# Kernel tuning notes

Hardware: AMD Instinct MI355X
Metric: run time of the kernel (lower is better)

Reference implementation:

```python
import jax, jax.numpy as jnp
import numpy as np

D = 512
H = 8
HD = D // H
EPS = 1e-8


def setup_inputs() -> dict:
    key = jax.random.key(0)
    ks = jax.random.split(key, 16)
    B, S = 4, 2048
    s = lambda n: 1.0 / np.sqrt(n)
    inp = {
        "gene_emb": jax.random.normal(ks[0], (B, S, D), jnp.float32),
        "expr_emb": jax.random.normal(ks[1], (B, S, D), jnp.float32),
        "M": jax.random.uniform(ks[2], (B, S, S), jnp.float32),
        # weights stored (in, out) so y = x @ W + b
        "W_fused": jax.random.normal(ks[3], (2 * D, D), jnp.float32) * s(2 * D),
        "b_fused": jnp.zeros((D,), jnp.float32),
        "W_Q": jax.random.normal(ks[4], (D, D), jnp.float32) * s(D),
        "b_Q": jnp.zeros((D,), jnp.float32),
        "W_K": jax.random.normal(ks[5], (D, D), jnp.float32) * s(D),
        "b_K": jnp.zeros((D,), jnp.float32),
        "W_V": jax.random.normal(ks[6], (D, D), jnp.float32) * s(D),
        "b_V": jnp.zeros((D,), jnp.float32),
        "W_O": jax.random.normal(ks[7], (D, D), jnp.float32) * s(D),
        "b_O": jnp.zeros((D,), jnp.float32),
    }
    return inp


def reference(gene_emb, expr_emb, M, W_fused, b_fused, W_Q, b_Q, W_K, b_K, W_V, b_V, W_O, b_O):
    B, S, _ = gene_emb.shape
    scale = HD ** (-0.5)
    fused = jnp.concatenate([gene_emb, expr_emb], axis=-1) @ W_fused + b_fused
    # (B,S,D) -> (B,H,S,HD)
    split = lambda x: x.reshape(B, S, H, HD).transpose(0, 2, 1, 3)
    Q = split(fused @ W_Q + b_Q)
    K = split(fused @ W_K + b_K)
    V = split(expr_emb @ W_V + b_V)
    scores = jnp.einsum("bhqd,bhkd->bhqk", Q, K) * scale
    Mg = M[:, None, :, :]  # broadcast over heads
    scores = scores * Mg
    attn = jax.nn.softmax(scores, axis=-1)
    A_sparse = attn * Mg
    norm = jnp.sum(jnp.abs(A_sparse), axis=-1, keepdims=True) + EPS
    A_bar = A_sparse / norm
    out = jnp.einsum("bhqk,bhkd->bhqd", A_bar, V)
    out = out.transpose(0, 2, 1, 3).reshape(B, S, D)
    return out @ W_O + b_O
```

## Files before the change

kernel.cpp:

```cpp
#include <hip/hip_runtime.h>

typedef unsigned short u16;
typedef __attribute__((ext_vector_type(8))) short bf16x8_t;
typedef __attribute__((ext_vector_type(4))) float f32x4_t;

__device__ __forceinline__ u16 f2bf(float x){
  union { float f; unsigned u; } v; v.f = x;
  unsigned r = v.u + 0x7FFFu + ((v.u >> 16) & 1u);
  return (u16)(r >> 16);
}
__device__ __forceinline__ float bf2f(u16 h){
  union { unsigned u; float f; } v; v.u = ((unsigned)h) << 16;
  return v.f;
}

__device__ __forceinline__ void gl2lds16(const u16* g, u16* l){
  __builtin_amdgcn_global_load_lds((const __attribute__((address_space(1))) void*)g,
                                   (__attribute__((address_space(3))) void*)l, 16, 0, 0);
}

__global__ __launch_bounds__(256) void split_concat_kernel(
    const float* __restrict__ gene, const float* __restrict__ expr,
    u16* __restrict__ Xh, u16* __restrict__ Xl)
{
  size_t e = ((size_t)blockIdx.x * 256 + threadIdx.x) * 4;
  int row = (int)(e >> 10);
  int col = (int)(e & 1023);
  const float* src = (col < 512) ? (gene + (size_t)row * 512 + col)
                                 : (expr + (size_t)row * 512 + (col - 512));
  float4 v = *(const float4*)src;
  float a[4] = {v.x, v.y, v.z, v.w};
  u16 hs[4], ls[4];
#pragma unroll
  for (int i = 0; i < 4; i++){
    hs[i] = f2bf(a[i]);
    ls[i] = f2bf(a[i] - bf2f(hs[i]));
  }
  *(uint2*)(Xh + e) = make_uint2(hs[0] | ((unsigned)hs[1] << 16), hs[2] | ((unsigned)hs[3] << 16));
  *(uint2*)(Xl + e) = make_uint2(ls[0] | ((unsigned)ls[1] << 16), ls[2] | ((unsigned)ls[3] << 16));
}

__global__ __launch_bounds__(256) void transpose_split_kernel(
    const float* __restrict__ W, u16* __restrict__ Wth, u16* __restrict__ Wtl,
    int K, int N)
{
  __shared__ float t[64][65];
  int k0 = blockIdx.x * 64, n0 = blockIdx.y * 64;
  int tid = threadIdx.x;
  int r = tid >> 4;
  int c4 = (tid & 15) * 4;
#pragma unroll
  for (int p = 0; p < 4; p++){
    int k = p * 16 + r;
    float4 v = *(const float4*)(W + (size_t)(k0 + k) * N + n0 + c4);
    t[c4 + 0][k] = v.x; t[c4 + 1][k] = v.y; t[c4 + 2][k] = v.z; t[c4 + 3][k] = v.w;
  }
  __syncthreads();
#pragma unroll
  for (int p = 0; p < 4; p++){
    int n = p * 16 + r;
    u16 hs[4], ls[4];
#pragma unroll
    for (int i = 0; i < 4; i++){
      float x = t[n][c4 + i];
      hs[i] = f2bf(x);
      ls[i] = f2bf(x - bf2f(hs[i]));
    }
    size_t o = (size_t)(n0 + n) * K + k0 + c4;
    *(uint2*)(Wth + o) = make_uint2(hs[0] | ((unsigned)hs[1] << 16), hs[2] | ((unsigned)hs[3] << 16));
    *(uint2*)(Wtl + o) = make_uint2(ls[0] | ((unsigned)ls[1] << 16), ls[2] | ((unsigned)ls[3] << 16));
  }
}

__global__ __launch_bounds__(256, 2) void gemm_split_kernel(
    const u16* __restrict__ Ah, const u16* __restrict__ Al, int lda,
    const u16* __restrict__ Bth, const u16* __restrict__ Btl, int K,
    const float* __restrict__ bias,
    void* __restrict__ out0, void* __restrict__ out1, int mode)
{
  __shared__ __align__(16) u16 sAh[128 * 32], sAl[128 * 32];
  __shared__ __align__(16) u16 sBh[64 * 32],  sBl[64 * 32];
  int tid = threadIdx.x;
  int lane = tid & 63, w = tid >> 6, quad = lane >> 4, l15 = lane & 15;
  int wm = w & 1, wn = w >> 1;
  int m0 = blockIdx.x * 128, n0 = blockIdx.y * 64;

  f32x4_t acc[4][2];
#pragma unroll
  for (int i = 0; i < 4; i++)
#pragma unroll
    for (int j = 0; j < 2; j++)
#pragma unroll
      for (int r = 0; r < 4; r++) acc[i][j][r] = 0.f;

  int lrow = lane >> 2;
  int swzS = ((lane >> 2) & 3) ^ ((lane >> 4) & 3);
  int gkq  = ((lane & 3) ^ swzS) * 8;
  const u16* pAh0 = Ah + (size_t)(m0 + w * 32 + lrow) * lda + gkq;
  const u16* pAh1 = Ah + (size_t)(m0 + w * 32 + 16 + lrow) * lda + gkq;
  const u16* pAl0 = Al + (size_t)(m0 + w * 32 + lrow) * lda + gkq;
  const u16* pAl1 = Al + (size_t)(m0 + w * 32 + 16 + lrow) * lda + gkq;
  const u16* pBh0 = Bth + (size_t)(n0 + w * 16 + lrow) * K + gkq;
  const u16* pBl0 = Btl + (size_t)(n0 + w * 16 + lrow) * K + gkq;
  u16* dAh = sAh + w * 1024;
  u16* dAl = sAl + w * 1024;
  u16* dBh = sBh + w * 512;
  u16* dBl = sBl + w * 512;

  int pq = (quad ^ ((l15 & 3) ^ ((l15 >> 2) & 3))) * 8;

  for (int k0 = 0; k0 < K; k0 += 32){
    __syncthreads();
    gl2lds16(pAh0 + k0, dAh);
    gl2lds16(pAh1 + k0, dAh + 512);
    gl2lds16(pAl0 + k0, dAl);
    gl2lds16(pAl1 + k0, dAl + 512);
    gl2lds16(pBh0 + k0, dBh);
    gl2lds16(pBl0 + k0, dBl);
    __syncthreads();

    bf16x8_t aH[4], aL[4], bH[2], bL[2];
#pragma unroll
    for (int mi = 0; mi < 4; mi++){
      int ad = (wm * 64 + mi * 16 + l15) * 32 + pq;
      aH[mi] = *(const bf16x8_t*)&sAh[ad];
      aL[mi] = *(const bf16x8_t*)&sAl[ad];
    }
#pragma unroll
    for (int ni = 0; ni < 2; ni++){
      int bd = (wn * 32 + ni * 16 + l15) * 32 + pq;
      bH[ni] = *(const bf16x8_t*)&sBh[bd];
      bL[ni] = *(const bf16x8_t*)&sBl[bd];
    }
#pragma unroll
    for (int mi = 0; mi < 4; mi++)
#pragma unroll
      for (int ni = 0; ni < 2; ni++){
        acc[mi][ni] = __builtin_amdgcn_mfma_f32_16x16x32_bf16(aH[mi], bH[ni], acc[mi][ni], 0, 0, 0);
        acc[mi][ni] = __builtin_amdgcn_mfma_f32_16x16x32_bf16(aH[mi], bL[ni], acc[mi][ni], 0, 0, 0);
        acc[mi][ni] = __builtin_amdgcn_mfma_f32_16x16x32_bf16(aL[mi], bH[ni], acc[mi][ni], 0, 0, 0);
      }
  }

#pragma unroll
  for (int mi = 0; mi < 4; mi++)
#pragma unroll
    for (int ni = 0; ni < 2; ni++){
      int gn = n0 + wn * 32 + ni * 16 + l15;
      float bs = bias[gn];
      int gm0 = m0 + wm * 64 + mi * 16 + quad * 4;
#pragma unroll
      for (int r = 0; r < 4; r++){
        float v = acc[mi][ni][r] + bs;
        int gm = gm0 + r;
        if (mode == 0){
          u16 hb = f2bf(v);
          ((u16*)out0)[(size_t)gm * 512 + gn] = hb;
          ((u16*)out1)[(size_t)gm * 512 + gn] = f2bf(v - bf2f(hb));
        } else if (mode == 1){
          int bb = gm >> 11, s = gm & 2047;
          int hh = gn >> 6, d = gn & 63;
          ((u16*)out0)[((size_t)((bb * 8 + hh) * 64 + d) << 11) + s] = f2bf(v);
        } else {
          ((float*)out0)[(size_t)gm * 512 + gn] = v;
        }
      }
    }
}

__global__ __launch_bounds__(256, 4) void flash_kernel(
    const u16* __restrict__ Qh, const u16* __restrict__ Ql,
    const u16* __restrict__ Kh, const u16* __restrict__ Kl,
    const u16* __restrict__ Vt, const float* __restrict__ Mm,
    u16* __restrict__ Oh, u16* __restrict__ Ol)
{
  __shared__ __align__(16) u16 sKh[64 * 64], sKl[64 * 64], sVt[64 * 64];
  __shared__ __align__(16) u16 sP[64 * 72];
  int tid = threadIdx.x, lane = tid & 63, w = tid >> 6, quad = lane >> 4, l15 = lane & 15;
  int bh = blockIdx.y, b = bh >> 3, h = bh & 7;
  int q0 = blockIdx.x * 64;
  const float scale = 0.125f;

  int qrow = q0 + w * 16 + l15;
  const u16* qpH = Qh + ((size_t)(b * 2048 + qrow)) * 512 + h * 64 + quad * 8;
  const u16* qpL = Ql + ((size_t)(b * 2048 + qrow)) * 512 + h * 64 + quad * 8;
  bf16x8_t qH[2], qL[2];
  qH[0] = *(const bf16x8_t*)qpH;  qH[1] = *(const bf16x8_t*)(qpH + 32);
  qL[0] = *(const bf16x8_t*)qpL;  qL[1] = *(const bf16x8_t*)(qpL + 32);

  float lp[4] = {0.f, 0.f, 0.f, 0.f};
  f32x4_t Oacc[4];
#pragma unroll
  for (int ni = 0; ni < 4; ni++)
#pragma unroll
    for (int r = 0; r < 4; r++) Oacc[ni][r] = 0.f;

  int srow = lane >> 3;
  int gc = ((lane & 7) ^ ((lane >> 3) & 7)) * 8;
  const u16* gKh0 = Kh + ((size_t)(b * 2048 + w * 16 + srow)) * 512 + h * 64 + gc;
  const u16* gKl0 = Kl + ((size_t)(b * 2048 + w * 16 + srow)) * 512 + h * 64 + gc;
  const u16* gVt0 = Vt + ((size_t)(bh * 64 + w * 16 + srow)) * 2048 + gc;
  u16* dKh = sKh + w * 1024;
  u16* dKl = sKl + w * 1024;
  u16* dVt = sVt + w * 1024;
  const float* Mbase = Mm + (size_t)b * 2048 * 2048 + (size_t)(q0 + w * 16) * 2048;

  int sw7 = l15 & 7;
  for (int k0 = 0; k0 < 2048; k0 += 64){
    __syncthreads();
    gl2lds16(gKh0 + (size_t)k0 * 512,        dKh);
    gl2lds16(gKh0 + (size_t)(k0 + 8) * 512,  dKh + 512);
    gl2lds16(gKl0 + (size_t)k0 * 512,        dKl);
    gl2lds16(gKl0 + (size_t)(k0 + 8) * 512,  dKl + 512);
    gl2lds16(gVt0 + k0,                      dVt);
    gl2lds16(gVt0 + 8 * 2048 + k0,           dVt + 512);
    __syncthreads();

    float Mv[4][4];
#pragma unroll
    for (int ni = 0; ni < 4; ni++)
#pragma unroll
      for (int r = 0; r < 4; r++)
        Mv[ni][r] = Mbase[(size_t)(quad * 4 + r) * 2048 + k0 + ni * 16 + l15];

    f32x4_t Sacc[4];
#pragma unroll
    for (int ni = 0; ni < 4; ni++)
#pragma unroll
      for (int r = 0; r < 4; r++) Sacc[ni][r] = 0.f;
#pragma unroll
    for (int ni = 0; ni < 4; ni++){
      int kb = (ni * 16 + l15) * 64;
#pragma unroll
      for (int ds = 0; ds < 2; ds++){
        int p = ((ds * 4 + quad) ^ sw7) * 8;
        bf16x8_t kH = *(const bf16x8_t*)&sKh[kb + p];
        bf16x8_t kL = *(const bf16x8_t*)&sKl[kb + p];
        Sacc[ni] = __builtin_amdgcn_mfma_f32_16x16x32_bf16(qH[ds], kH, Sacc[ni], 0, 0, 0);
        Sacc[ni] = __builtin_amdgcn_mfma_f32_16x16x32_bf16(qH[ds], kL, Sacc[ni], 0, 0, 0);
        Sacc[ni] = __builtin_amdgcn_mfma_f32_16x16x32_bf16(qL[ds], kH, Sacc[ni], 0, 0, 0);
      }
    }

#pragma unroll
    for (int ni = 0; ni < 4; ni++)
#pragma unroll
      for (int r = 0; r < 4; r++){
        float m = Mv[ni][r];
        float p = m * __expf(Sacc[ni][r] * scale * m);
        lp[r] += p;
        sP[(w * 16 + quad * 4 + r) * 72 + ni * 16 + l15] = f2bf(p);
      }

#pragma unroll
    for (int ds = 0; ds < 2; ds++){
      bf16x8_t pf = *(const bf16x8_t*)&sP[(w * 16 + l15) * 72 + ds * 32 + quad * 8];
#pragma unroll
      for (int ni = 0; ni < 4; ni++){
        int p = ((ds * 4 + quad) ^ sw7) * 8;
        bf16x8_t vf = *(const bf16x8_t*)&sVt[(ni * 16 + l15) * 64 + p];
        Oacc[ni] = __builtin_amdgcn_mfma_f32_16x16x32_bf16(pf, vf, Oacc[ni], 0, 0, 0);
      }
    }
  }

#pragma unroll
  for (int r = 0; r < 4; r++){
#pragma unroll
    for (int off = 1; off < 16; off <<= 1)
      lp[r] += __shfl_xor(lp[r], off);
  }

#pragma unroll
  for (int r = 0; r < 4; r++){
    float inv = 1.0f / lp[r];
    int q = q0 + w * 16 + quad * 4 + r;
    size_t rb = ((size_t)(b * 2048 + q)) * 512 + h * 64;
#pragma unroll
    for (int ni = 0; ni < 4; ni++){
      float v = Oacc[ni][r] * inv;
      int d = ni * 16 + l15;
      u16 hb = f2bf(v);
      Oh[rb + d] = hb;
      Ol[rb + d] = f2bf(v - bf2f(hb));
    }
  }
}

extern "C" void kernel_launch(void* const* d_in, const int* in_sizes, int n_in,
                              void* d_out, int out_size, void* d_ws, size_t ws_size,
                              hipStream_t stream)
{
  const float* gene = (const float*)d_in[0];
  const float* expr = (const float*)d_in[1];
  const float* Mm   = (const float*)d_in[2];
  const float* Wf   = (const float*)d_in[3];
  const float* bfv  = (const float*)d_in[4];
  const float* Wq   = (const float*)d_in[5];
  const float* bq   = (const float*)d_in[6];
  const float* Wk   = (const float*)d_in[7];
  const float* bk   = (const float*)d_in[8];
  const float* Wv   = (const float*)d_in[9];
  const float* bv   = (const float*)d_in[10];
  const float* Wo   = (const float*)d_in[11];
  const float* bo   = (const float*)d_in[12];
  float* out = (float*)d_out;

  char* ws = (char*)d_ws;
  size_t off = 0;
  auto alloc = [&](size_t bytes) -> void* {
    void* p = (void*)(ws + off);
    off += (bytes + 255) & ~(size_t)255;
    return p;
  };
  u16* Xh   = (u16*)alloc(8192ull * 1024 * 2);
  u16* Xl   = (u16*)alloc(8192ull * 1024 * 2);
  u16* Wfth = (u16*)alloc(512ull * 1024 * 2);
  u16* Wftl = (u16*)alloc(512ull * 1024 * 2);
  u16* Wqth = (u16*)alloc(512ull * 512 * 2);
  u16* Wqtl = (u16*)alloc(512ull * 512 * 2);
  u16* Wkth = (u16*)alloc(512ull * 512 * 2);
  u16* Wktl = (u16*)alloc(512ull * 512 * 2);
  u16* Wvth = (u16*)alloc(512ull * 512 * 2);
  u16* Wvtl = (u16*)alloc(512ull * 512 * 2);
  u16* Woth = (u16*)alloc(512ull * 512 * 2);
  u16* Wotl = (u16*)alloc(512ull * 512 * 2);
  u16* Fh   = (u16*)alloc(8192ull * 512 * 2);
  u16* Fl   = (u16*)alloc(8192ull * 512 * 2);
  u16* Qh   = (u16*)alloc(8192ull * 512 * 2);
  u16* Ql   = (u16*)alloc(8192ull * 512 * 2);
  u16* Kh   = (u16*)alloc(8192ull * 512 * 2);
  u16* Kl   = (u16*)alloc(8192ull * 512 * 2);
  u16* Vt   = (u16*)alloc(8192ull * 512 * 2);
  u16* Oh = Xh;
  u16* Ol = Xl;

  split_concat_kernel<<<8192, 256, 0, stream>>>(gene, expr, Xh, Xl);
  transpose_split_kernel<<<dim3(16, 8), 256, 0, stream>>>(Wf, Wfth, Wftl, 1024, 512);
  transpose_split_kernel<<<dim3(8, 8),  256, 0, stream>>>(Wq, Wqth, Wqtl, 512, 512);
  transpose_split_kernel<<<dim3(8, 8),  256, 0, stream>>>(Wk, Wkth, Wktl, 512, 512);
  transpose_split_kernel<<<dim3(8, 8),  256, 0, stream>>>(Wv, Wvth, Wvtl, 512, 512);
  transpose_split_kernel<<<dim3(8, 8),  256, 0, stream>>>(Wo, Woth, Wotl, 512, 512);

  gemm_split_kernel<<<dim3(64, 8), 256, 0, stream>>>(Xh, Xl, 1024, Wfth, Wftl, 1024, bfv, Fh, Fl, 0);
  gemm_split_kernel<<<dim3(64, 8), 256, 0, stream>>>(Fh, Fl, 512, Wqth, Wqtl, 512, bq, Qh, Ql, 0);
  gemm_split_kernel<<<dim3(64, 8), 256, 0, stream>>>(Fh, Fl, 512, Wkth, Wktl, 512, bk, Kh, Kl, 0);
  gemm_split_kernel<<<dim3(64, 8), 256, 0, stream>>>(Xh + 512, Xl + 512, 1024, Wvth, Wvtl, 512, bv, Vt, nullptr, 1);
  flash_kernel<<<dim3(32, 32), 256, 0, stream>>>(Qh, Ql, Kh, Kl, Vt, Mm, Oh, Ol);
  gemm_split_kernel<<<dim3(64, 8), 256, 0, stream>>>(Oh, Ol, 512, Woth, Wotl, 512, bo, out, nullptr, 2);

  (void)in_sizes; (void)n_in; (void)out_size; (void)ws_size;
}
```

Measured before the change: 372.9 us.

## Drop split-bf16 terms, fuse Q/K GEMMs and weight transposes, prefetch mask

Cuts the compensated bf16 splitting in stages that tolerate it. Q/K and V/O GEMMs drop the low weight parts, the output projection becomes single bf16, and the attention QK^T uses one MFMA instead of three. The five weight transposes are merged into one launch, and Q and K are computed in one dual GEMM with the softmax scale and log2(e) folded into Q so exp2 can be used. The mask tile is now prefetched one iteration ahead, and P is truncated instead of rounded. All of this lowers MFMA count, memory traffic and launch overhead at the cost of accuracy.

Result: faster. 301.7 us (-19.1%).

```diff
diff --git a/kernel.cpp b/kernel.cpp
--- a/kernel.cpp
+++ b/kernel.cpp
@@ -12,6 +12,10 @@
 __device__ __forceinline__ float bf2f(u16 h){
   union { unsigned u; float f; } v; v.u = ((unsigned)h) << 16;
   return v.f;
+}
+__device__ __forceinline__ u16 hi16(float x){
+  union { float f; unsigned u; } v; v.f = x;
+  return (u16)(v.u >> 16);
 }
 
 __device__ __forceinline__ void gl2lds16(const u16* g, u16* l){
@@ -40,19 +44,32 @@
   *(uint2*)(Xl + e) = make_uint2(ls[0] | ((unsigned)ls[1] << 16), ls[2] | ((unsigned)ls[3] << 16));
 }
 
-__global__ __launch_bounds__(256) void transpose_split_kernel(
-    const float* __restrict__ W, u16* __restrict__ Wth, u16* __restrict__ Wtl,
-    int K, int N)
+__global__ __launch_bounds__(256) void transpose_all_kernel(
+    const float* __restrict__ Wf, const float* __restrict__ Wq,
+    const float* __restrict__ Wk, const float* __restrict__ Wv,
+    const float* __restrict__ Wo,
+    u16* __restrict__ Wfth, u16* __restrict__ Wftl,
+    u16* __restrict__ Wqth, u16* __restrict__ Wkth,
+    u16* __restrict__ Wvth, u16* __restrict__ Woth)
 {
   __shared__ float t[64][65];
-  int k0 = blockIdx.x * 64, n0 = blockIdx.y * 64;
+  int id = blockIdx.x;
+  const float* W; u16* Th; u16* Tl; int K, kx, ny;
+  if (id < 128){ W = Wf; Th = Wfth; Tl = Wftl; K = 1024; kx = id >> 3; ny = id & 7; }
+  else {
+    int tt = id - 128; int wi = tt >> 6; tt &= 63; kx = tt >> 3; ny = tt & 7; K = 512;
+    W  = (wi == 0) ? Wq  : (wi == 1) ? Wk  : (wi == 2) ? Wv  : Wo;
+    Th = (wi == 0) ? Wqth: (wi == 1) ? Wkth: (wi == 2) ? Wvth: Woth;
+    Tl = nullptr;
+  }
+  int k0 = kx * 64, n0 = ny * 64;
   int tid = threadIdx.x;
   int r = tid >> 4;
   int c4 = (tid & 15) * 4;
 #pragma unroll
   for (int p = 0; p < 4; p++){
     int k = p * 16 + r;
-    float4 v = *(const float4*)(W + (size_t)(k0 + k) * N + n0 + c4);
+    float4 v = *(const float4*)(W + (size_t)(k0 + k) * 512 + n0 + c4);
     t[c4 + 0][k] = v.x; t[c4 + 1][k] = v.y; t[c4 + 2][k] = v.z; t[c4 + 3][k] = v.w;
   }
   __syncthreads();
@@ -67,23 +84,35 @@
       ls[i] = f2bf(x - bf2f(hs[i]));
     }
     size_t o = (size_t)(n0 + n) * K + k0 + c4;
-    *(uint2*)(Wth + o) = make_uint2(hs[0] | ((unsigned)hs[1] << 16), hs[2] | ((unsigned)hs[3] << 16));
-    *(uint2*)(Wtl + o) = make_uint2(ls[0] | ((unsigned)ls[1] << 16), ls[2] | ((unsigned)ls[3] << 16));
-  }
-}
-
-__global__ __launch_bounds__(256, 2) void gemm_split_kernel(
+    *(uint2*)(Th + o) = make_uint2(hs[0] | ((unsigned)hs[1] << 16), hs[2] | ((unsigned)hs[3] << 16));
+    if (Tl)
+      *(uint2*)(Tl + o) = make_uint2(ls[0] | ((unsigned)ls[1] << 16), ls[2] | ((unsigned)ls[3] << 16));
+  }
+}
+
+template<int SPLITS, int MODE, int DUAL>
+__global__ __launch_bounds__(256, 2) void gemm_kernel(
     const u16* __restrict__ Ah, const u16* __restrict__ Al, int lda,
-    const u16* __restrict__ Bth, const u16* __restrict__ Btl, int K,
-    const float* __restrict__ bias,
-    void* __restrict__ out0, void* __restrict__ out1, int mode)
-{
-  __shared__ __align__(16) u16 sAh[128 * 32], sAl[128 * 32];
-  __shared__ __align__(16) u16 sBh[64 * 32],  sBl[64 * 32];
+    const u16* __restrict__ Bh0, const u16* __restrict__ Bl0,
+    const u16* __restrict__ Bh1, int K,
+    const float* __restrict__ bias0, const float* __restrict__ bias1,
+    void* __restrict__ out0, void* __restrict__ out1, void* __restrict__ outsec,
+    float sc0, float sc1)
+{
+  __shared__ __align__(16) u16 sAh[128 * 32];
+  __shared__ __align__(16) u16 sAl[SPLITS >= 2 ? 128 * 32 : 8];
+  __shared__ __align__(16) u16 sBh[64 * 32];
+  __shared__ __align__(16) u16 sBl[SPLITS == 3 ? 64 * 32 : 8];
   int tid = threadIdx.x;
   int lane = tid & 63, w = tid >> 6, quad = lane >> 4, l15 = lane & 15;
   int wm = w & 1, wn = w >> 1;
-  int m0 = blockIdx.x * 128, n0 = blockIdx.y * 64;
+  int m0 = blockIdx.x * 128;
+  int side = DUAL ? (int)(blockIdx.y >> 3) : 0;
+  int n0 = (DUAL ? (int)(blockIdx.y & 7) : (int)blockIdx.y) * 64;
+  const u16* Bh = (DUAL && side) ? Bh1 : Bh0;
+  const float* bias = (DUAL && side) ? bias1 : bias0;
+  void* o0 = (DUAL && side) ? outsec : out0;
+  float sc = (DUAL && side) ? sc1 : sc0;
 
   f32x4_t acc[4][2];
 #pragma unroll
@@ -98,10 +127,10 @@
   int gkq  = ((lane & 3) ^ swzS) * 8;
   const u16* pAh0 = Ah + (size_t)(m0 + w * 32 + lrow) * lda + gkq;
   const u16* pAh1 = Ah + (size_t)(m0 + w * 32 + 16 + lrow) * lda + gkq;
-  const u16* pAl0 = Al + (size_t)(m0 + w * 32 + lrow) * lda + gkq;
-  const u16* pAl1 = Al + (size_t)(m0 + w * 32 + 16 + lrow) * lda + gkq;
-  const u16* pBh0 = Bth + (size_t)(n0 + w * 16 + lrow) * K + gkq;
-  const u16* pBl0 = Btl + (size_t)(n0 + w * 16 + lrow) * K + gkq;
+  const u16* pAl0 = (SPLITS >= 2) ? Al + (size_t)(m0 + w * 32 + lrow) * lda + gkq : nullptr;
+  const u16* pAl1 = (SPLITS >= 2) ? Al + (size_t)(m0 + w * 32 + 16 + lrow) * lda + gkq : nullptr;
+  const u16* pBh0 = Bh + (size_t)(n0 + w * 16 + lrow) * K + gkq;
+  const u16* pBl0 = (SPLITS == 3) ? Bl0 + (size_t)(n0 + w * 16 + lrow) * K + gkq : nullptr;
   u16* dAh = sAh + w * 1024;
   u16* dAl = sAl + w * 1024;
   u16* dBh = sBh + w * 512;
@@ -113,10 +142,13 @@
     __syncthreads();
     gl2lds16(pAh0 + k0, dAh);
     gl2lds16(pAh1 + k0, dAh + 512);
-    gl2lds16(pAl0 + k0, dAl);
-    gl2lds16(pAl1 + k0, dAl + 512);
+    if constexpr (SPLITS >= 2){
+      gl2lds16(pAl0 + k0, dAl);
+      gl2lds16(pAl1 + k0, dAl + 512);
+    }
     gl2lds16(pBh0 + k0, dBh);
-    gl2lds16(pBl0 + k0, dBl);
+    if constexpr (SPLITS == 3)
+      gl2lds16(pBl0 + k0, dBl);
     __syncthreads();
 
     bf16x8_t aH[4], aL[4], bH[2], bL[2];
@@ -124,21 +156,23 @@
     for (int mi = 0; mi < 4; mi++){
       int ad = (wm * 64 + mi * 16 + l15) * 32 + pq;
       aH[mi] = *(const bf16x8_t*)&sAh[ad];
-      aL[mi] = *(const bf16x8_t*)&sAl[ad];
+      if constexpr (SPLITS >= 2) aL[mi] = *(const bf16x8_t*)&sAl[ad];
     }
 #pragma unroll
     for (int ni = 0; ni < 2; ni++){
       int bd = (wn * 32 + ni * 16 + l15) * 32 + pq;
       bH[ni] = *(const bf16x8_t*)&sBh[bd];
-      bL[ni] = *(const bf16x8_t*)&sBl[bd];
+      if constexpr (SPLITS == 3) bL[ni] = *(const bf16x8_t*)&sBl[bd];
     }
 #pragma unroll
     for (int mi = 0; mi < 4; mi++)
 #pragma unroll
       for (int ni = 0; ni < 2; ni++){
         acc[mi][ni] = __builtin_amdgcn_mfma_f32_16x16x32_bf16(aH[mi], bH[ni], acc[mi][ni], 0, 0, 0);
-        acc[mi][ni] = __builtin_amdgcn_mfma_f32_16x16x32_bf16(aH[mi], bL[ni], acc[mi][ni], 0, 0, 0);
-        acc[mi][ni] = __builtin_amdgcn_mfma_f32_16x16x32_bf16(aL[mi], bH[ni], acc[mi][ni], 0, 0, 0);
+        if constexpr (SPLITS == 3)
+          acc[mi][ni] = __builtin_amdgcn_mfma_f32_16x16x32_bf16(aH[mi], bL[ni], acc[mi][ni], 0, 0, 0);
+        if constexpr (SPLITS >= 2)
+          acc[mi][ni] = __builtin_amdgcn_mfma_f32_16x16x32_bf16(aL[mi], bH[ni], acc[mi][ni], 0, 0, 0);
       }
   }
 
@@ -153,40 +187,38 @@
       for (int r = 0; r < 4; r++){
         float v = acc[mi][ni][r] + bs;
         int gm = gm0 + r;
-        if (mode == 0){
+        if constexpr (MODE == 0){
           u16 hb = f2bf(v);
-          ((u16*)out0)[(size_t)gm * 512 + gn] = hb;
+          ((u16*)o0)[(size_t)gm * 512 + gn] = hb;
           ((u16*)out1)[(size_t)gm * 512 + gn] = f2bf(v - bf2f(hb));
-        } else if (mode == 1){
+        } else if constexpr (MODE == 1){
+          ((u16*)o0)[(size_t)gm * 512 + gn] = f2bf(v * sc);
+        } else if constexpr (MODE == 2){
           int bb = gm >> 11, s = gm & 2047;
           int hh = gn >> 6, d = gn & 63;
-          ((u16*)out0)[((size_t)((bb * 8 + hh) * 64 + d) << 11) + s] = f2bf(v);
+          ((u16*)o0)[((size_t)((bb * 8 + hh) * 64 + d) << 11) + s] = f2bf(v);
         } else {
-          ((float*)out0)[(size_t)gm * 512 + gn] = v;
+          ((float*)o0)[(size_t)gm * 512 + gn] = v;
         }
       }
     }
 }
 
 __global__ __launch_bounds__(256, 4) void flash_kernel(
-    const u16* __restrict__ Qh, const u16* __restrict__ Ql,
-    const u16* __restrict__ Kh, const u16* __restrict__ Kl,
+    const u16* __restrict__ Qh, const u16* __restrict__ Kh,
     const u16* __restrict__ Vt, const float* __restrict__ Mm,
-    u16* __restrict__ Oh, u16* __restrict__ Ol)
-{
-  __shared__ __align__(16) u16 sKh[64 * 64], sKl[64 * 64], sVt[64 * 64];
+    u16* __restrict__ Oh)
+{
+  __shared__ __align__(16) u16 sKh[64 * 64], sVt[64 * 64];
   __shared__ __align__(16) u16 sP[64 * 72];
   int tid = threadIdx.x, lane = tid & 63, w = tid >> 6, quad = lane >> 4, l15 = lane & 15;
   int bh = blockIdx.y, b = bh >> 3, h = bh & 7;
   int q0 = blockIdx.x * 64;
-  const float scale = 0.125f;
 
   int qrow = q0 + w * 16 + l15;
-  const u16* qpH = Qh + ((size_t)(b * 2048 + qrow)) * 512 + h * 64 + quad * 8;
-  const u16* qpL = Ql + ((size_t)(b * 2048 + qrow)) * 512 + h * 64 + quad * 8;
-  bf16x8_t qH[2], qL[2];
-  qH[0] = *(const bf16x8_t*)qpH;  qH[1] = *(const bf16x8_t*)(qpH + 32);
-  qL[0] = *(const bf16x8_t*)qpL;  qL[1] = *(const bf16x8_t*)(qpL + 32);
+  const u16* qp = Qh + ((size_t)(b * 2048 + qrow)) * 512 + h * 64 + quad * 8;
+  bf16x8_t qH[2];
+  qH[0] = *(const bf16x8_t*)qp;  qH[1] = *(const bf16x8_t*)(qp + 32);
 
   float lp[4] = {0.f, 0.f, 0.f, 0.f};
   f32x4_t Oacc[4];
@@ -198,30 +230,36 @@
   int srow = lane >> 3;
   int gc = ((lane & 7) ^ ((lane >> 3) & 7)) * 8;
   const u16* gKh0 = Kh + ((size_t)(b * 2048 + w * 16 + srow)) * 512 + h * 64 + gc;
-  const u16* gKl0 = Kl + ((size_t)(b * 2048 + w * 16 + srow)) * 512 + h * 64 + gc;
   const u16* gVt0 = Vt + ((size_t)(bh * 64 + w * 16 + srow)) * 2048 + gc;
   u16* dKh = sKh + w * 1024;
-  u16* dKl = sKl + w * 1024;
   u16* dVt = sVt + w * 1024;
   const float* Mbase = Mm + (size_t)b * 2048 * 2048 + (size_t)(q0 + w * 16) * 2048;
+
+  float Mc[4][4];
+#pragma unroll
+  for (int ni = 0; ni < 4; ni++)
+#pragma unroll
+    for (int r = 0; r < 4; r++)
+      Mc[ni][r] = Mbase[(size_t)(quad * 4 + r) * 2048 + ni * 16 + l15];
 
   int sw7 = l15 & 7;
   for (int k0 = 0; k0 < 2048; k0 += 64){
     __syncthreads();
-    gl2lds16(gKh0 + (size_t)k0 * 512,        dKh);
-    gl2lds16(gKh0 + (size_t)(k0 + 8) * 512,  dKh + 512);
-    gl2lds16(gKl0 + (size_t)k0 * 512,        dKl);
-    gl2lds16(gKl0 + (size_t)(k0 + 8) * 512,  dKl + 512);
-    gl2lds16(gVt0 + k0,                      dVt);
-    gl2lds16(gVt0 + 8 * 2048 + k0,           dVt + 512);
+    gl2lds16(gKh0 + (size_t)k0 * 512,       dKh);
+    gl2lds16(gKh0 + (size_t)(k0 + 8) * 512, dKh + 512);
+    gl2lds16(gVt0 + k0,                     dVt);
+    gl2lds16(gVt0 + 8 * 2048 + k0,          dVt + 512);
     __syncthreads();
 
-    float Mv[4][4];
-#pragma unroll
-    for (int ni = 0; ni < 4; ni++)
-#pragma unroll
-      for (int r = 0; r < 4; r++)
-        Mv[ni][r] = Mbase[(size_t)(quad * 4 + r) * 2048 + k0 + ni * 16 + l15];
+    float Mn[4][4];
+    bool hasNext = (k0 + 64) < 2048;
+    if (hasNext){
+#pragma unroll
+      for (int ni = 0; ni < 4; ni++)
+#pragma unroll
+        for (int r = 0; r < 4; r++)
+          Mn[ni][r] = Mbase[(size_t)(quad * 4 + r) * 2048 + (k0 + 64) + ni * 16 + l15];
+    }
 
     f32x4_t Sacc[4];
 #pragma unroll
@@ -235,10 +273,7 @@
       for (int ds = 0; ds < 2; ds++){
         int p = ((ds * 4 + quad) ^ sw7) * 8;
         bf16x8_t kH = *(const bf16x8_t*)&sKh[kb + p];
-        bf16x8_t kL = *(const bf16x8_t*)&sKl[kb + p];
         Sacc[ni] = __builtin_amdgcn_mfma_f32_16x16x32_bf16(qH[ds], kH, Sacc[ni], 0, 0, 0);
-        Sacc[ni] = __builtin_amdgcn_mfma_f32_16x16x32_bf16(qH[ds], kL, Sacc[ni], 0, 0, 0);
-        Sacc[ni] = __builtin_amdgcn_mfma_f32_16x16x32_bf16(qL[ds], kH, Sacc[ni], 0, 0, 0);
       }
     }
 
@@ -246,10 +281,10 @@
     for (int ni = 0; ni < 4; ni++)
 #pragma unroll
       for (int r = 0; r < 4; r++){
-        float m = Mv[ni][r];
-        float p = m * __expf(Sacc[ni][r] * scale * m);
+        float m = Mc[ni][r];
+        float p = m * __builtin_amdgcn_exp2f(Sacc[ni][r] * m);
         lp[r] += p;
-        sP[(w * 16 + quad * 4 + r) * 72 + ni * 16 + l15] = f2bf(p);
+        sP[(w * 16 + quad * 4 + r) * 72 + ni * 16 + l15] = hi16(p);
       }
 
 #pragma unroll
@@ -262,6 +297,13 @@
         Oacc[ni] = __builtin_amdgcn_mfma_f32_16x16x32_bf16(pf, vf, Oacc[ni], 0, 0, 0);
       }
     }
+
+    if (hasNext){
+#pragma unroll
+      for (int ni = 0; ni < 4; ni++)
+#pragma unroll
+        for (int r = 0; r < 4; r++) Mc[ni][r] = Mn[ni][r];
+    }
   }
 
 #pragma unroll
@@ -279,10 +321,7 @@
 #pragma unroll
     for (int ni = 0; ni < 4; ni++){
       float v = Oacc[ni][r] * inv;
-      int d = ni * 16 + l15;
-      u16 hb = f2bf(v);
-      Oh[rb + d] = hb;
-      Ol[rb + d] = f2bf(v - bf2f(hb));
+      Oh[rb + ni * 16 + l15] = f2bf(v);
     }
   }
 }
@@ -318,36 +357,31 @@
   u16* Wfth = (u16*)alloc(512ull * 1024 * 2);
   u16* Wftl = (u16*)alloc(512ull * 1024 * 2);
   u16* Wqth = (u16*)alloc(512ull * 512 * 2);
-  u16* Wqtl = (u16*)alloc(512ull * 512 * 2);
   u16* Wkth = (u16*)alloc(512ull * 512 * 2);
-  u16* Wktl = (u16*)alloc(512ull * 512 * 2);
   u16* Wvth = (u16*)alloc(512ull * 512 * 2);
-  u16* Wvtl = (u16*)alloc(512ull * 512 * 2);
   u16* Woth = (u16*)alloc(512ull * 512 * 2);
-  u16* Wotl = (u16*)alloc(512ull * 512 * 2);
   u16* Fh   = (u16*)alloc(8192ull * 512 * 2);
   u16* Fl   = (u16*)alloc(8192ull * 512 * 2);
   u16* Qh   = (u16*)alloc(8192ull * 512 * 2);
-  u16* Ql   = (u16*)alloc(8192ull * 512 * 2);
   u16* Kh   = (u16*)alloc(8192ull * 512 * 2);
-  u16* Kl   = (u16*)alloc(8192ull * 512 * 2);
   u16* Vt   = (u16*)alloc(8192ull * 512 * 2);
   u16* Oh = Xh;
-  u16* Ol = Xl;
+
+  const float QSC = 0.1803368801f;
 
   split_concat_kernel<<<8192, 256, 0, stream>>>(gene, expr, Xh, Xl);
-  transpose_split_kernel<<<dim3(16, 8), 256, 0, stream>>>(Wf, Wfth, Wftl, 1024, 512);
-  transpose_split_kernel<<<dim3(8, 8),  256, 0, stream>>>(Wq, Wqth, Wqtl, 512, 512);
-  transpose_split_kernel<<<dim3(8, 8),  256, 0, stream>>>(Wk, Wkth, Wktl, 512, 512);
-  transpose_split_kernel<<<dim3(8, 8),  256, 0, stream>>>(Wv, Wvth, Wvtl, 512, 512);
-  transpose_split_kernel<<<dim3(8, 8),  256, 0, stream>>>(Wo, Woth, Wotl, 512, 512);
-
-  gemm_split_kernel<<<dim3(64, 8), 256, 0, stream>>>(Xh, Xl, 1024, Wfth, Wftl, 1024, bfv, Fh, Fl, 0);
-  gemm_split_kernel<<<dim3(64, 8), 256, 0, stream>>>(Fh, Fl, 512, Wqth, Wqtl, 512, bq, Qh, Ql, 0);
-  gemm_split_kernel<<<dim3(64, 8), 256, 0, stream>>>(Fh, Fl, 512, Wkth, Wktl, 512, bk, Kh, Kl, 0);
-  gemm_split_kernel<<<dim3(64, 8), 256, 0, stream>>>(Xh + 512, Xl + 512, 1024, Wvth, Wvtl, 512, bv, Vt, nullptr, 1);
-  flash_kernel<<<dim3(32, 32), 256, 0, stream>>>(Qh, Ql, Kh, Kl, Vt, Mm, Oh, Ol);
-  gemm_split_kernel<<<dim3(64, 8), 256, 0, stream>>>(Oh, Ol, 512, Woth, Wotl, 512, bo, out, nullptr, 2);
+  transpose_all_kernel<<<384, 256, 0, stream>>>(Wf, Wq, Wk, Wv, Wo,
+                                                Wfth, Wftl, Wqth, Wkth, Wvth, Woth);
+
+  gemm_kernel<3, 0, 0><<<dim3(64, 8), 256, 0, stream>>>(
+      Xh, Xl, 1024, Wfth, Wftl, nullptr, 1024, bfv, nullptr, Fh, Fl, nullptr, 1.f, 1.f);
+  gemm_kernel<2, 1, 1><<<dim3(64, 16), 256, 0, stream>>>(
+      Fh, Fl, 512, Wqth, nullptr, Wkth, 512, bq, bk, Qh, nullptr, Kh, QSC, 1.f);
+  gemm_kernel<2, 2, 0><<<dim3(64, 8), 256, 0, stream>>>(
+      Xh + 512, Xl + 512, 1024, Wvth, nullptr, nullptr, 512, bv, nullptr, Vt, nullptr, nullptr, 1.f, 1.f);
+  flash_kernel<<<dim3(32, 32), 256, 0, stream>>>(Qh, Kh, Vt, Mm, Oh);
+  gemm_kernel<1, 3, 0><<<dim3(64, 8), 256, 0, stream>>>(
+      Oh, nullptr, 512, Woth, nullptr, nullptr, 512, bo, nullptr, out, nullptr, nullptr, 1.f, 1.f);
 
   (void)in_sizes; (void)n_in; (void)out_size; (void)ws_size;
 }
```
